# Performance work log

Measured on AMD Instinct MI355X. Metric: run time of the kernel, lower is better.

Reference implementation:

```python
import jax, jax.numpy as jnp
import numpy as np

B, S, E, KD = 4, 2048, 1024, 1024

def setup_inputs() -> dict:
    key = jax.random.key(0)
    k1, k2, k3, k4 = jax.random.split(key, 4)
    # nn.Linear weights are [out_features, in_features]
    x = jax.random.normal(k1, (B, S, E), dtype=jnp.float32)
    W_q = jax.random.normal(k2, (KD, E), dtype=jnp.float32) * (E ** -0.5)
    W_k = jax.random.normal(k3, (KD, E), dtype=jnp.float32) * (E ** -0.5)
    W_v = jax.random.normal(k4, (E, E), dtype=jnp.float32) * (E ** -0.5)
    return {"x": x, "W_q": W_q, "W_k": W_k, "W_v": W_v}

def reference(x, W_q, W_k, W_v):
    # Projections: y = x @ W.T  (torch Linear convention)
    Q = jnp.einsum('bse,ke->bsk', x, W_q)   # [B,S,KD]
    K = jnp.einsum('bse,ke->bsk', x, W_k)   # [B,S,KD]
    V = jnp.einsum('bse,fe->bsf', x, W_v)   # [B,S,E]
    key_dim = W_q.shape[0]
    scores = jnp.einsum('bqk,bsk->bqs', Q, K) / jnp.sqrt(jnp.asarray(key_dim, x.dtype))
    S_len = x.shape[1]
    causal = jnp.tril(jnp.ones((S_len, S_len), dtype=bool))  # [S,S]
    scores = jnp.where(causal, scores, -jnp.inf)
    weights = jax.nn.softmax(scores, axis=-1)                # [B,S,S]
    out = jnp.einsum('bqs,bsf->bqf', weights, V)             # [B,S,E]
    return out
```

## Files before the change

### kernel.cpp

```cpp
#include <hip/hip_runtime.h>

typedef _Float16 f16;
typedef _Float16 f16x8 __attribute__((ext_vector_type(8)));
typedef float    f32x4 __attribute__((ext_vector_type(4)));

__device__ __forceinline__ void gld_lds16(const void* g, void* l) {
    __builtin_amdgcn_global_load_lds((__attribute__((address_space(1))) void*)g,
                                     (__attribute__((address_space(3))) void*)l,
                                     16, 0, 0);
}

template<typename OutT, int MODE>
__global__ void __launch_bounds__(256)
gemm_bt(const f16* __restrict__ A, const f16* __restrict__ B, OutT* __restrict__ C,
        int lda, int ldb, int ldc, int K, float scale,
        long sA, long sB, long sC)
{
    const int bz = blockIdx.z;
    A += (long)bz * sA;
    B += (long)bz * sB;
    C += (long)bz * sC;

    int bx = blockIdx.x, by = blockIdx.y;
    if (MODE == 1) {
        const int t = bx;
        int y = 0;
        while ((y + 1) * (y + 2) <= t) y++;
        by = y;
        bx = t - y * (y + 1);
    }
    if (MODE == 2 && (blockIdx.z & 2)) by = (int)gridDim.y - 1 - by;

    const int i0 = by * 128;
    const int j0 = bx * 64;
    int Keff = K;
    if (MODE == 2) Keff = min(K, i0 + 128);

    __shared__ f16 As[128 * 64] __attribute__((aligned(16)));
    __shared__ f16 Bs[64 * 64]  __attribute__((aligned(16)));

    const int tid  = threadIdx.x;
    const int lane = tid & 63;
    const int wave = tid >> 6;
    const int row16 = lane & 15;
    const int quad  = lane >> 4;
    const int swz   = row16 & 7;
    const int wr = (wave >> 1) * 64;
    const int wc = (wave & 1) * 32;

    const int srow = tid >> 3;
    const int scol = ((tid & 7) ^ (srow & 7)) * 8;
    const f16* gA = A + (long)(i0 + srow) * lda + scol;
    const f16* gB = B + (long)(j0 + srow) * ldb + scol;
    f16* lA = As + tid * 8;
    f16* lB = Bs + tid * 8;

    f32x4 acc[4][2] = {};

    for (int k0 = 0; k0 < Keff; k0 += 64) {
        gld_lds16(gA + k0,                  lA);
        gld_lds16(gA + k0 + (long)32 * lda, lA + 32 * 64);
        gld_lds16(gA + k0 + (long)64 * lda, lA + 64 * 64);
        gld_lds16(gA + k0 + (long)96 * lda, lA + 96 * 64);
        gld_lds16(gB + k0,                  lB);
        gld_lds16(gB + k0 + (long)32 * ldb, lB + 32 * 64);
        __syncthreads();

        #pragma unroll
        for (int kk = 0; kk < 2; kk++) {
            f16x8 af[4], bf[2];
            #pragma unroll
            for (int t = 0; t < 4; t++)
                af[t] = *(const f16x8*)(As + (wr + t * 16 + row16) * 64
                                           + (((kk * 4 + quad) ^ swz) * 8));
            #pragma unroll
            for (int t = 0; t < 2; t++)
                bf[t] = *(const f16x8*)(Bs + (wc + t * 16 + row16) * 64
                                           + (((kk * 4 + quad) ^ swz) * 8));
            #pragma unroll
            for (int mt = 0; mt < 4; mt++)
                #pragma unroll
                for (int nt = 0; nt < 2; nt++)
                    acc[mt][nt] = __builtin_amdgcn_mfma_f32_16x16x32_f16(
                        af[mt], bf[nt], acc[mt][nt], 0, 0, 0);
        }
        __syncthreads();
    }

    #pragma unroll
    for (int mt = 0; mt < 4; mt++) {
        const int r0 = i0 + wr + mt * 16 + quad * 4;
        #pragma unroll
        for (int nt = 0; nt < 2; nt++) {
            const int c = j0 + wc + nt * 16 + row16;
            #pragma unroll
            for (int r = 0; r < 4; r++)
                C[(long)(r0 + r) * ldc + c] = (OutT)(acc[mt][nt][r] * scale);
        }
    }
}

__global__ void __launch_bounds__(256)
softmax_causal(f16* __restrict__ Sc)
{
    const int S = 2048;
    const long rowg = blockIdx.x;
    const long b = rowg >> 11;
    const int  i = (int)(rowg & 2047);
    f16* row = Sc + ((b * S + i) * (long)S);
    const int L = ((i >> 7) + 1) << 7;

    const int tid = threadIdx.x;
    const int c0  = tid * 8;
    const int lane = tid & 63, wave = tid >> 6;
    const bool act = c0 < L;

    float v[8];
    float m = -3.4e38f;
    if (act) {
        f16x8 in = *(const f16x8*)(row + c0);
        #pragma unroll
        for (int j = 0; j < 8; j++) {
            const bool ok = (c0 + j) <= i;
            v[j] = ok ? (float)in[j] : -3.4e38f;
            m = fmaxf(m, v[j]);
        }
    }
    #pragma unroll
    for (int off = 32; off > 0; off >>= 1)
        m = fmaxf(m, __shfl_down(m, off, 64));
    __shared__ float redm[4];
    if (lane == 0) redm[wave] = m;
    __syncthreads();
    const float m0 = fmaxf(fmaxf(redm[0], redm[1]), fmaxf(redm[2], redm[3]));

    float e[8];
    float s = 0.f;
    if (act) {
        #pragma unroll
        for (int j = 0; j < 8; j++) {
            const bool ok = (c0 + j) <= i;
            e[j] = ok ? __expf(v[j] - m0) : 0.f;
            s += e[j];
        }
    }
    #pragma unroll
    for (int off = 32; off > 0; off >>= 1)
        s += __shfl_down(s, off, 64);
    __shared__ float reds[4];
    if (lane == 0) reds[wave] = s;
    __syncthreads();
    const float inv = 1.f / (reds[0] + reds[1] + reds[2] + reds[3]);

    if (act) {
        f16x8 o;
        #pragma unroll
        for (int j = 0; j < 8; j++) o[j] = (f16)(e[j] * inv);
        *(f16x8*)(row + c0) = o;
    }
}

__global__ void __launch_bounds__(256)
convert_all(const float* __restrict__ x, const float* __restrict__ Wq,
            const float* __restrict__ Wk, const float* __restrict__ Wv,
            f16* __restrict__ xh, f16* __restrict__ wh)
{
    const long blk = blockIdx.x;
    const float* src;
    f16* dst;
    long base;
    if (blk < 4096)      { src = x;  dst = xh;                    base = blk * 2048; }
    else if (blk < 4608) { src = Wq; dst = wh;                    base = (blk - 4096) * 2048; }
    else if (blk < 5120) { src = Wk; dst = wh + 1024L * 1024;     base = (blk - 4608) * 2048; }
    else                 { src = Wv; dst = wh + 2L * 1024 * 1024; base = (blk - 5120) * 2048; }
    const long i = base + (long)threadIdx.x * 8;
    f32x4 a = *(const f32x4*)(src + i);
    f32x4 b = *(const f32x4*)(src + i + 4);
    f16x8 o;
    o[0] = (f16)a[0]; o[1] = (f16)a[1]; o[2] = (f16)a[2]; o[3] = (f16)a[3];
    o[4] = (f16)b[0]; o[5] = (f16)b[1]; o[6] = (f16)b[2]; o[7] = (f16)b[3];
    *(f16x8*)(dst + i) = o;
}

extern "C" void kernel_launch(void* const* d_in, const int* in_sizes, int n_in,
                              void* d_out, int out_size, void* d_ws, size_t ws_size,
                              hipStream_t stream)
{
    (void)in_sizes; (void)n_in; (void)out_size; (void)ws_size;
    const float* x  = (const float*)d_in[0];
    const float* Wq = (const float*)d_in[1];
    const float* Wk = (const float*)d_in[2];
    const float* Wv = (const float*)d_in[3];
    float* out = (float*)d_out;

    const long NX = 4L * 2048 * 1024;
    const long NW = 1024L * 1024;

    char* p = (char*)d_ws;
    f16* xh  = (f16*)p; p += NX * 2;
    f16* wh  = (f16*)p; p += 3 * NW * 2;
    f16* QKh = (f16*)p; p += 2 * NX * 2;
    f16* Vt  = (f16*)p; p += NX * 2;
    f16* Sc  = (f16*)p; p += 4L * 2048 * 2048 * 2;
    f16* wvh = wh + 2L * NW;

    convert_all<<<5632, 256, 0, stream>>>(x, Wq, Wk, Wv, xh, wh);

    gemm_bt<f16, 0><<<dim3(32, 64, 1), 256, 0, stream>>>(
        xh, wh, QKh, 1024, 1024, 2048, 1024, 1.f, 0, 0, 0);
    gemm_bt<f16, 0><<<dim3(128, 8, 1), 256, 0, stream>>>(
        wvh, xh, Vt, 1024, 1024, 8192, 1024, 1.f, 0, 0, 0);

    gemm_bt<f16, 1><<<dim3(272, 1, 4), 256, 0, stream>>>(
        QKh, QKh + 1024, Sc, 2048, 2048, 2048, 1024, 0.03125f,
        2048L * 2048, 2048L * 2048, 2048L * 2048);

    softmax_causal<<<4 * 2048, 256, 0, stream>>>(Sc);

    gemm_bt<float, 2><<<dim3(16, 16, 4), 256, 0, stream>>>(
        Sc, Vt, out, 2048, 8192, 1024, 2048, 1.f,
        2048L * 2048, 2048L, 2048L * 1024);
}
```

Before: 247.0 us.

## Add 256x256 double-buffered GEMM for fused Q/K projection

Replaces the 128x64 single-buffered GEMM used for the Q/K projection with a new 256x256-tile, 512-thread kernel specialised for K=1024. It double-buffers LDS and interleaves global-to-LDS loads with MFMA phases, using explicit waitcnts, barriers and setprio to overlap memory with compute. Larger tiles raise operand reuse per LDS byte. The trade-off is only 256 blocks (about one wave of blocks on the GPU), 128 KB of LDS per block, high register pressure, and fragile hand-placed synchronisation.

```diff
diff --git a/kernel.cpp b/kernel.cpp
--- a/kernel.cpp
+++ b/kernel.cpp
@@ -8,6 +8,166 @@
     __builtin_amdgcn_global_load_lds((__attribute__((address_space(1))) void*)g,
                                      (__attribute__((address_space(3))) void*)l,
                                      16, 0, 0);
+}
+
+#define BARRIER() do { asm volatile("" ::: "memory"); \
+                       __builtin_amdgcn_s_barrier();  \
+                       asm volatile("" ::: "memory"); } while (0)
+
+template<bool SB, bool SA, int VM>
+__device__ __forceinline__ void tile256(
+    f32x4 (&acc)[8][4],
+    const f16* Ak0, const f16* Ak1, const f16* Bk0, const f16* Bk1,
+    const f16* gBn, f16* lBn,
+    const f16* gAn, f16* lAn,
+    int lda, int ldb)
+{
+    f16x8 a0[8], a1[8], b0[4], b1[4];
+    #pragma unroll
+    for (int mf = 0; mf < 8; mf++) a0[mf] = *(const f16x8*)(Ak0 + mf * 1024);
+    #pragma unroll
+    for (int nf = 0; nf < 4; nf++) b0[nf] = *(const f16x8*)(Bk0 + nf * 1024);
+    if (SB) {
+        gld_lds16(gBn,                  lBn);
+        gld_lds16(gBn + (long)64 * ldb, lBn + 4096);
+    }
+    BARRIER();
+    __builtin_amdgcn_s_setprio(1);
+    #pragma unroll
+    for (int mf = 0; mf < 4; mf++)
+        #pragma unroll
+        for (int nf = 0; nf < 4; nf++)
+            acc[mf][nf] = __builtin_amdgcn_mfma_f32_16x16x32_f16(
+                a0[mf], b0[nf], acc[mf][nf], 0, 0, 0);
+    __builtin_amdgcn_s_setprio(0);
+    BARRIER();
+    #pragma unroll
+    for (int mf = 0; mf < 8; mf++) a1[mf] = *(const f16x8*)(Ak1 + mf * 1024);
+    #pragma unroll
+    for (int nf = 0; nf < 4; nf++) b1[nf] = *(const f16x8*)(Bk1 + nf * 1024);
+    if (SB) {
+        gld_lds16(gBn + (long)128 * ldb, lBn + 8192);
+        gld_lds16(gBn + (long)192 * ldb, lBn + 12288);
+    }
+    BARRIER();
+    __builtin_amdgcn_s_setprio(1);
+    #pragma unroll
+    for (int mf = 4; mf < 8; mf++)
+        #pragma unroll
+        for (int nf = 0; nf < 4; nf++)
+            acc[mf][nf] = __builtin_amdgcn_mfma_f32_16x16x32_f16(
+                a0[mf], b0[nf], acc[mf][nf], 0, 0, 0);
+    __builtin_amdgcn_s_setprio(0);
+    asm volatile("s_waitcnt lgkmcnt(0)" ::: "memory");
+    BARRIER();
+    if (SA) {
+        gld_lds16(gAn,                  lAn);
+        gld_lds16(gAn + (long)64 * lda, lAn + 4096);
+    }
+    BARRIER();
+    __builtin_amdgcn_s_setprio(1);
+    #pragma unroll
+    for (int mf = 0; mf < 4; mf++)
+        #pragma unroll
+        for (int nf = 0; nf < 4; nf++)
+            acc[mf][nf] = __builtin_amdgcn_mfma_f32_16x16x32_f16(
+                a1[mf], b1[nf], acc[mf][nf], 0, 0, 0);
+    __builtin_amdgcn_s_setprio(0);
+    BARRIER();
+    if (SA) {
+        gld_lds16(gAn + (long)128 * lda, lAn + 8192);
+        gld_lds16(gAn + (long)192 * lda, lAn + 12288);
+    }
+    BARRIER();
+    __builtin_amdgcn_s_setprio(1);
+    #pragma unroll
+    for (int mf = 4; mf < 8; mf++)
+        #pragma unroll
+        for (int nf = 0; nf < 4; nf++)
+            acc[mf][nf] = __builtin_amdgcn_mfma_f32_16x16x32_f16(
+                a1[mf], b1[nf], acc[mf][nf], 0, 0, 0);
+    __builtin_amdgcn_s_setprio(0);
+    if (VM == 4)      asm volatile("s_waitcnt vmcnt(4)" ::: "memory");
+    else if (VM == 0) asm volatile("s_waitcnt vmcnt(0)" ::: "memory");
+    BARRIER();
+}
+
+__global__ void __launch_bounds__(512, 2)
+gemm256_k1024(const f16* __restrict__ A, const f16* __restrict__ B,
+              f16* __restrict__ C, int lda, int ldb, int ldc)
+{
+    const int i0 = blockIdx.y * 256;
+    const int j0 = blockIdx.x * 256;
+
+    __shared__ f16 L[2 * 32768] __attribute__((aligned(16)));
+
+    const int tid  = threadIdx.x;
+    const int lane = tid & 63;
+    const int wave = tid >> 6;
+    const int wm = wave >> 2, wn = wave & 3;
+    const int row16 = lane & 15, quad = lane >> 4;
+    const int swz = row16 & 7;
+
+    const int c0 = (quad ^ swz) * 8;
+    const int c1 = ((quad + 4) ^ swz) * 8;
+    const f16* A0k0 = L + (wm * 128 + row16) * 64 + c0;
+    const f16* A0k1 = L + (wm * 128 + row16) * 64 + c1;
+    const f16* B0k0 = L + 16384 + (wn * 64 + row16) * 64 + c0;
+    const f16* B0k1 = L + 16384 + (wn * 64 + row16) * 64 + c1;
+
+    const int srow = tid >> 3;
+    const int scol = ((tid & 7) ^ (srow & 7)) * 8;
+    const f16* gA = A + (long)(i0 + srow) * lda + scol;
+    const f16* gB = B + (long)(j0 + srow) * ldb + scol;
+    f16* lA0 = L + tid * 8;
+    f16* lB0 = L + 16384 + tid * 8;
+    f16* lA1 = L + 32768 + tid * 8;
+    f16* lB1 = L + 32768 + 16384 + tid * 8;
+
+    gld_lds16(gA,                   lA0);
+    gld_lds16(gA + (long)64 * lda,  lA0 + 4096);
+    gld_lds16(gA + (long)128 * lda, lA0 + 8192);
+    gld_lds16(gA + (long)192 * lda, lA0 + 12288);
+    gld_lds16(gB,                   lB0);
+    gld_lds16(gB + (long)64 * ldb,  lB0 + 4096);
+    gld_lds16(gB + (long)128 * ldb, lB0 + 8192);
+    gld_lds16(gB + (long)192 * ldb, lB0 + 12288);
+    gld_lds16(gA + 64,                   lA1);
+    gld_lds16(gA + 64 + (long)64 * lda,  lA1 + 4096);
+    gld_lds16(gA + 64 + (long)128 * lda, lA1 + 8192);
+    gld_lds16(gA + 64 + (long)192 * lda, lA1 + 12288);
+
+    f32x4 acc[8][4] = {};
+
+    asm volatile("s_waitcnt vmcnt(4)" ::: "memory");
+    BARRIER();
+
+    for (int t = 0; t < 14; t += 2) {
+        tile256<true, true, 4>(acc, A0k0, A0k1, B0k0, B0k1,
+                               gB + (t + 1) * 64, lB1,
+                               gA + (t + 2) * 64, lA0, lda, ldb);
+        tile256<true, true, 4>(acc, A0k0 + 32768, A0k1 + 32768,
+                               B0k0 + 32768, B0k1 + 32768,
+                               gB + (t + 2) * 64, lB0,
+                               gA + (t + 3) * 64, lA1, lda, ldb);
+    }
+    tile256<true, false, 0>(acc, A0k0, A0k1, B0k0, B0k1,
+                            gB + 15 * 64, lB1, nullptr, nullptr, lda, ldb);
+    tile256<false, false, -1>(acc, A0k0 + 32768, A0k1 + 32768,
+                              B0k0 + 32768, B0k1 + 32768,
+                              nullptr, nullptr, nullptr, nullptr, lda, ldb);
+
+    #pragma unroll
+    for (int mf = 0; mf < 8; mf++) {
+        const int r0 = i0 + wm * 128 + mf * 16 + quad * 4;
+        #pragma unroll
+        for (int nf = 0; nf < 4; nf++) {
+            const int c = j0 + wn * 64 + nf * 16 + row16;
+            #pragma unroll
+            for (int r = 0; r < 4; r++)
+                C[(long)(r0 + r) * ldc + c] = (f16)acc[mf][nf][r];
+        }
+    }
 }
 
 template<typename OutT, int MODE>
@@ -206,8 +366,8 @@
 
     convert_all<<<5632, 256, 0, stream>>>(x, Wq, Wk, Wv, xh, wh);
 
-    gemm_bt<f16, 0><<<dim3(32, 64, 1), 256, 0, stream>>>(
-        xh, wh, QKh, 1024, 1024, 2048, 1024, 1.f, 0, 0, 0);
+    gemm256_k1024<<<dim3(8, 32, 1), 512, 0, stream>>>(
+        xh, wh, QKh, 1024, 1024, 2048);
     gemm_bt<f16, 0><<<dim3(128, 8, 1), 256, 0, stream>>>(
         wvh, xh, Vt, 1024, 1024, 8192, 1024, 1.f, 0, 0, 0);
 
```

New measurement: 248.2 us. About the same (+0.5%).
